# Kernel optimization log

Hardware: AMD Instinct MI355X
Metric: run time of the kernel (lower is better)

The kernel has to match this reference:

```python
import jax, jax.numpy as jnp
import numpy as np

N, D, DH, H = 2048, 256, 256, 4
DHEAD = DH // H
NEG = -1e30


def setup_inputs() -> dict:
    key = jax.random.key(0)
    ks = jax.random.split(key, 24)
    s = 0.05
    inp = {
        'axiom_states': jax.random.normal(ks[0], (N, D), jnp.float32),
        'adj0': (jax.random.uniform(ks[1], (N, N)) < 0.015).astype(jnp.float32),
        'adj1': (jax.random.uniform(ks[2], (N, N)) < 0.015).astype(jnp.float32),
        'w0': jax.random.uniform(ks[3], (N, N), jnp.float32),
        'w1': jax.random.uniform(ks[4], (N, N), jnp.float32),
        'Wm0': jax.random.normal(ks[5], (DH, D), jnp.float32) * s,
        'bm0': jax.random.normal(ks[6], (DH,), jnp.float32) * s,
        'Wa0': jax.random.normal(ks[7], (H, 2 * D), jnp.float32) * s,
        'ba0': jax.random.normal(ks[8], (H,), jnp.float32) * s,
        'Wm1': jax.random.normal(ks[9], (DH, D), jnp.float32) * s,
        'bm1': jax.random.normal(ks[10], (DH,), jnp.float32) * s,
        'Wa1': jax.random.normal(ks[11], (H, 2 * D), jnp.float32) * s,
        'ba1': jax.random.normal(ks[12], (H,), jnp.float32) * s,
        'gru_wih': jax.random.normal(ks[13], (3 * D, 2 * DH), jnp.float32) * s,
        'gru_whh': jax.random.normal(ks[14], (3 * D, D), jnp.float32) * s,
        'gru_bih': jax.random.normal(ks[15], (3 * D,), jnp.float32) * s,
        'gru_bhh': jax.random.normal(ks[16], (3 * D,), jnp.float32) * s,
        'ln_g': jnp.ones((D,), jnp.float32),
        'ln_b': jnp.zeros((D,), jnp.float32),
    }
    return inp


def _edge_messages(x, adj, w, Wm, bm, Wa, ba):
    # GAT-style decomposition of Linear([x_i, x_j]) -> a_cur[i] + a_nb[j] + b
    a_cur = x @ Wa[:, :D].T                      # [N,H] (target i, first half of concat)
    a_nb = x @ Wa[:, D:].T                       # [N,H] (neighbor j, second half)
    s = a_nb[:, None, :] + a_cur[None, :, :] + ba  # [j,i,H]
    s = jax.nn.leaky_relu(s, 0.2)
    s = s * w[:, :, None]                        # edge-weight scaled scores (pre-softmax)
    mask = adj != 0                              # edge j -> i iff adj[j,i] != 0
    logits = jnp.where(mask[:, :, None], s, NEG)
    attn = jax.nn.softmax(logits, axis=0) * mask[:, :, None]  # zero for isolated nodes
    msg = (x @ Wm.T + bm).reshape(N, H, DHEAD)   # per-neighbor messages
    agg = jnp.einsum('jih,jhd->ihd', attn, msg)  # softmax-weighted sum over neighbors
    return agg.reshape(N, DH)


def _forward(axiom_states, adj0, adj1, w0, w1, Wm0, bm0, Wa0, ba0,
             Wm1, bm1, Wa1, ba1, gru_wih, gru_whh, gru_bih, gru_bhh, ln_g, ln_b):
    m0 = _edge_messages(axiom_states, adj0, w0, Wm0, bm0, Wa0, ba0)
    m1 = _edge_messages(axiom_states, adj1, w1, Wm1, bm1, Wa1, ba1)
    msg = jnp.concatenate([m0, m1], axis=-1)     # dropout is identity in eval
    # GRUCell (torch semantics)
    gi = msg @ gru_wih.T + gru_bih
    gh = axiom_states @ gru_whh.T + gru_bhh
    r = jax.nn.sigmoid(gi[:, :D] + gh[:, :D])
    z = jax.nn.sigmoid(gi[:, D:2 * D] + gh[:, D:2 * D])
    n = jnp.tanh(gi[:, 2 * D:] + r * gh[:, 2 * D:])
    h = (1.0 - z) * n + z * axiom_states
    # LayerNorm
    mu = jnp.mean(h, axis=-1, keepdims=True)
    var = jnp.var(h, axis=-1, keepdims=True)
    return (h - mu) * jax.lax.rsqrt(var + 1e-5) * ln_g + ln_b


def reference(axiom_states, adj0, adj1, w0, w1, Wm0, bm0, Wa0, ba0,
              Wm1, bm1, Wa1, ba1, gru_wih, gru_whh, gru_bih, gru_bhh, ln_g, ln_b):
    return _forward(axiom_states, adj0, adj1, w0, w1, Wm0, bm0, Wa0, ba0,
                    Wm1, bm1, Wa1, ba1, gru_wih, gru_whh, gru_bih, gru_bhh, ln_g, ln_b)
```

## Files before the change

kernel.cpp:

```cpp
#include <hip/hip_runtime.h>

#define NN 2048
#define DD 256
#define HH 4
#define ECAP 128

typedef unsigned short ushort_t;
typedef __attribute__((ext_vector_type(4))) unsigned short us4;
typedef __attribute__((ext_vector_type(8))) unsigned short us8;
typedef __attribute__((ext_vector_type(8))) short s8;
typedef __attribute__((ext_vector_type(4))) float f4;

__device__ __forceinline__ ushort_t f2b(float f) {
    unsigned int u = __float_as_uint(f);
    return (ushort_t)((u + 0x7fffu + ((u >> 16) & 1u)) >> 16);
}
__device__ __forceinline__ float b2f(ushort_t b) {
    return __uint_as_float(((unsigned int)b) << 16);
}
__device__ __forceinline__ void gl_lds16(const void* g, void* l) {
    __builtin_amdgcn_global_load_lds(
        (const __attribute__((address_space(1))) void*)g,
        (__attribute__((address_space(3))) void*)l, 16, 0, 0);
}

__device__ __forceinline__ us8 cvt8(float4 a, float4 b) {
    us8 o;
    o[0] = f2b(a.x); o[1] = f2b(a.y); o[2] = f2b(a.z); o[3] = f2b(a.w);
    o[4] = f2b(b.x); o[5] = f2b(b.y); o[6] = f2b(b.z); o[7] = f2b(b.w);
    return o;
}

__device__ __forceinline__ void gemm_core_f32(
    const float* __restrict__ A, int lda, const float* __restrict__ B, int ldb,
    int r0, int c0, int K, ushort_t (*as)[64], ushort_t (*bs)[64], f4 acc[2][2])
{
    const int t = threadIdx.x;
    const int wave = t >> 6, lane = t & 63;
    const int wm = (wave & 1) * 32, wn = (wave >> 1) * 32;
    const int fm = lane & 15, fq = lane >> 4;

    const int m1 = wave * 16 + (lane >> 3);
    const int m2 = m1 + 8;
    const int g1 = ((lane & 7) ^ (m1 & 7)) * 8;
    const int g2 = ((lane & 7) ^ (m2 & 7)) * 8;
    const int cl = (lane & 7) * 8;
    const int ra0 = wm + fm, ra1 = wm + 16 + fm;
    const int rb0 = wn + fm, rb1 = wn + 16 + fm;

    const float* pa1 = A + (size_t)(r0 + m1) * lda + g1;
    const float* pa2 = A + (size_t)(r0 + m2) * lda + g2;
    const float* pb1 = B + (size_t)(c0 + m1) * ldb + g1;
    const float* pb2 = B + (size_t)(c0 + m2) * ldb + g2;

    float4 aa0 = *(const float4*)(pa1);
    float4 aa1 = *(const float4*)(pa1 + 4);
    float4 ab0 = *(const float4*)(pa2);
    float4 ab1 = *(const float4*)(pa2 + 4);
    float4 ba0 = *(const float4*)(pb1);
    float4 ba1 = *(const float4*)(pb1 + 4);
    float4 bb0 = *(const float4*)(pb2);
    float4 bb1 = *(const float4*)(pb2 + 4);

    for (int k0 = 0; k0 < K; k0 += 64) {
        __syncthreads();
        *(us8*)&as[m1][cl] = cvt8(aa0, aa1);
        *(us8*)&as[m2][cl] = cvt8(ab0, ab1);
        *(us8*)&bs[m1][cl] = cvt8(ba0, ba1);
        *(us8*)&bs[m2][cl] = cvt8(bb0, bb1);
        __syncthreads();
        if (k0 + 64 < K) {
            aa0 = *(const float4*)(pa1 + k0 + 64);
            aa1 = *(const float4*)(pa1 + k0 + 68);
            ab0 = *(const float4*)(pa2 + k0 + 64);
            ab1 = *(const float4*)(pa2 + k0 + 68);
            ba0 = *(const float4*)(pb1 + k0 + 64);
            ba1 = *(const float4*)(pb1 + k0 + 68);
            bb0 = *(const float4*)(pb2 + k0 + 64);
            bb1 = *(const float4*)(pb2 + k0 + 68);
        }
        #pragma unroll
        for (int kk = 0; kk < 2; ++kk) {
            const int cc = kk * 4 + fq;
            const s8 a0 = *(const s8*)&as[ra0][(cc ^ (ra0 & 7)) * 8];
            const s8 a1 = *(const s8*)&as[ra1][(cc ^ (ra1 & 7)) * 8];
            const s8 b0 = *(const s8*)&bs[rb0][(cc ^ (rb0 & 7)) * 8];
            const s8 b1 = *(const s8*)&bs[rb1][(cc ^ (rb1 & 7)) * 8];
            acc[0][0] = __builtin_amdgcn_mfma_f32_16x16x32_bf16(a0, b0, acc[0][0], 0, 0, 0);
            acc[0][1] = __builtin_amdgcn_mfma_f32_16x16x32_bf16(a0, b1, acc[0][1], 0, 0, 0);
            acc[1][0] = __builtin_amdgcn_mfma_f32_16x16x32_bf16(a1, b0, acc[1][0], 0, 0, 0);
            acc[1][1] = __builtin_amdgcn_mfma_f32_16x16x32_bf16(a1, b1, acc[1][1], 0, 0, 0);
        }
    }
}

#define E_SC  256
#define E_AP  384
#define E_NB  1024

__global__ __launch_bounds__(256) void fused1_kernel(
    const float* __restrict__ x,
    const float* __restrict__ adj0, const float* __restrict__ adj1,
    const float* __restrict__ Wm0, const float* __restrict__ Wm1,
    const float* __restrict__ whh,
    const float* __restrict__ Wa0, const float* __restrict__ Wa1,
    const float* __restrict__ bm0, const float* __restrict__ bm1,
    const float* __restrict__ bhh,
    int* __restrict__ cnt, int* __restrict__ ej,
    float* __restrict__ acur, float* __restrict__ anb,
    ushort_t* __restrict__ msgb, float* __restrict__ gh)
{
    __shared__ char smem[16448];
    const int b = blockIdx.x, t = threadIdx.x;

    if (b < E_SC) {
        const int l = b & 1, chunk = b >> 1;
        const int i0 = chunk * 16;
        const float* adj = l ? adj1 : adj0;
        int* lcnt = (int*)smem;
        if (t < 16) lcnt[t] = 0;
        __syncthreads();
        const int rowLane = t >> 2, q = t & 3;
        for (int r0r = 0; r0r < NN; r0r += 512) {
            float4 a[8];
            #pragma unroll
            for (int it = 0; it < 8; ++it) {
                const int j = r0r + it * 64 + rowLane;
                a[it] = *(const float4*)(adj + (size_t)j * NN + i0 + q * 4);
            }
            #pragma unroll
            for (int it = 0; it < 8; ++it) {
                const int j = r0r + it * 64 + rowLane;
                const float av[4] = {a[it].x, a[it].y, a[it].z, a[it].w};
                #pragma unroll
                for (int u = 0; u < 4; ++u) {
                    if (av[u] != 0.f) {
                        const int li = q * 4 + u;
                        const int slot = atomicAdd(&lcnt[li], 1);
                        if (slot < ECAP)
                            ej[((size_t)l * NN + i0 + li) * ECAP + slot] = j;
                    }
                }
            }
        }
        __syncthreads();
        if (t < 16) cnt[l * NN + i0 + t] = min(lcnt[t], ECAP);
        return;
    }
    if (b < E_AP) {
        float* sh = (float*)smem;
        const int i0 = (b - E_SC) * 16;
        for (int rr = 0; rr < 16; ++rr)
            sh[rr * 257 + t] = x[(size_t)(i0 + rr) * DD + t];
        __syncthreads();
        const int r = t >> 4, idx = t & 15;
        const int l = idx >> 3, isnb = (idx >> 2) & 1, h = idx & 3;
        const float* wrow = (l ? Wa1 : Wa0) + h * (2 * DD) + isnb * DD;
        float acc = 0.f;
        for (int k = 0; k < DD; ++k) acc = fmaf(sh[r * 257 + k], wrow[k], acc);
        float* dst = isnb ? anb : acur;
        dst[((size_t)l * NN + i0 + r) * HH + h] = acc;
        return;
    }
    {
        ushort_t (*as)[64] = (ushort_t(*)[64])smem;
        ushort_t (*bs)[64] = (ushort_t(*)[64])(smem + 8192);
        const int wave = t >> 6, lane = t & 63;
        const int wm = (wave & 1) * 32, wn = (wave >> 1) * 32;
        const int fm = lane & 15, fq = lane >> 4;
        const int idx = b - E_AP;
        const int c0 = (idx % 20) * 64, r0 = (idx / 20) * 64;
        const float* Bsrc = (c0 < 256) ? Wm0 + (size_t)c0 * DD
                          : (c0 < 512) ? Wm1 + (size_t)(c0 - 256) * DD
                                       : whh + (size_t)(c0 - 512) * DD;
        f4 acc[2][2] = {};
        gemm_core_f32(x, DD, Bsrc, DD, r0, 0, DD, as, bs, acc);
        #pragma unroll
        for (int ni = 0; ni < 2; ++ni) {
            const int col = c0 + wn + ni * 16 + fm;
            const float bv = (col < 256) ? bm0[col]
                           : (col < 512) ? bm1[col - 256]
                                         : bhh[col - 512];
            #pragma unroll
            for (int mi = 0; mi < 2; ++mi) {
                #pragma unroll
                for (int r = 0; r < 4; ++r) {
                    const int row = r0 + wm + mi * 16 + fq * 4 + r;
                    const float v = acc[mi][ni][r] + bv;
                    if (col < 512) msgb[(size_t)row * 512 + col] = f2b(v);
                    else           gh[(size_t)row * 768 + col - 512] = v;
                }
            }
        }
    }
}

__global__ __launch_bounds__(256) void attn_kernel(
    const int* __restrict__ cnt, const int* __restrict__ ej,
    const float* __restrict__ w0, const float* __restrict__ w1,
    const float* __restrict__ acur, const float* __restrict__ anb,
    const float* __restrict__ ba0, const float* __restrict__ ba1,
    const ushort_t* __restrict__ msgb, ushort_t* __restrict__ mcatb,
    const float* __restrict__ wih, ushort_t* __restrict__ wihb)
{
    const int i = blockIdx.x, l = blockIdx.y, t = threadIdx.x;
    __shared__ float es[HH][ECAP];
    __shared__ int ejs[ECAP];

    {
        const int fb = i + (l << 11);
        if (t < 24) {
            const int id = fb * 96 + t * 4;
            const float4 v = *(const float4*)(wih + id);
            us4 o; o.x = f2b(v.x); o.y = f2b(v.y); o.z = f2b(v.z); o.w = f2b(v.w);
            *(us4*)(wihb + id) = o;
        }
    }

    const int ne = min(max(cnt[l * NN + i], 0), ECAP);
    const float* ba = l ? ba1 : ba0;
    const float* w  = l ? w1 : w0;
    const size_t ebase = ((size_t)l * NN + i) * ECAP;

    if (t < ne) {
        const int j = ej[ebase + t];
        const float wv = w[(size_t)j * NN + i];
        ejs[t] = j;
        const float4 av = *(const float4*)(anb + ((size_t)l * NN + j) * HH);
        const float sv[4] = {av.x, av.y, av.z, av.w};
        #pragma unroll
        for (int h = 0; h < HH; ++h) {
            float s = sv[h] + acur[((size_t)l * NN + i) * HH + h] + ba[h];
            s = (s > 0.f) ? s : 0.2f * s;
            es[h][t] = s * wv;
        }
    }
    __syncthreads();
    {
        const int h = t >> 6, lane = t & 63;
        float s0 = (lane < ne) ? es[h][lane] : -1e30f;
        float s1 = (lane + 64 < ne) ? es[h][lane + 64] : -1e30f;
        float m = fmaxf(s0, s1);
        #pragma unroll
        for (int off = 32; off; off >>= 1) m = fmaxf(m, __shfl_xor(m, off));
        const float p0 = expf(s0 - m), p1 = expf(s1 - m);
        float sum = p0 + p1;
        #pragma unroll
        for (int off = 32; off; off >>= 1) sum += __shfl_xor(sum, off);
        const float inv = (ne > 0) ? 1.f / sum : 0.f;
        es[h][lane] = p0 * inv;
        if (lane + 64 < ECAP) es[h][lane + 64] = p1 * inv;
    }
    __syncthreads();
    const int h = t >> 6;
    const int off = l * DD + t;
    float acc = 0.f;
    int e = 0;
    for (; e + 8 <= ne; e += 8) {
        float v[8];
        #pragma unroll
        for (int u = 0; u < 8; ++u)
            v[u] = b2f(msgb[(size_t)ejs[e + u] * 512 + off]);
        #pragma unroll
        for (int u = 0; u < 8; ++u)
            acc = fmaf(es[h][e + u], v[u], acc);
    }
    for (; e < ne; ++e)
        acc = fmaf(es[h][e], b2f(msgb[(size_t)ejs[e] * 512 + off]), acc);
    mcatb[(size_t)i * (2 * DD) + off] = f2b(acc);
}

__global__ __launch_bounds__(256) void gemm2_kernel(
    const ushort_t* __restrict__ mcatb, const ushort_t* __restrict__ wihb,
    const float* __restrict__ bih, float* __restrict__ gi)
{
    __shared__ ushort_t as[256][64];
    __shared__ ushort_t bs[128][64];
    const int t = threadIdx.x;
    const int wave = t >> 6, lane = t & 63;
    const int wm = wave * 32;
    const int fm = lane & 15, fq = lane >> 4;
    const int c0 = blockIdx.x * 64, r0 = blockIdx.y * 128;

    const int lr = lane >> 3;
    const int swz = ((lane & 7) ^ lr) * 8;
    const ushort_t* gaA[4];
    const ushort_t* gaB[2];
    #pragma unroll
    for (int g = 0; g < 4; ++g)
        gaA[g] = mcatb + (size_t)(r0 + wm + g * 8 + lr) * 512 + swz;
    #pragma unroll
    for (int g = 0; g < 2; ++g)
        gaB[g] = wihb + (size_t)(c0 + wave * 16 + g * 8 + lr) * 512 + swz;

    f4 acc[2][4] = {};

    #pragma unroll
    for (int g = 0; g < 4; ++g) gl_lds16(gaA[g], &as[wm + g * 8][0]);
    #pragma unroll
    for (int g = 0; g < 2; ++g) gl_lds16(gaB[g], &bs[wave * 16 + g * 8][0]);
    __syncthreads();

    int abuf = 0, bbuf = 0;
    for (int k0 = 0; k0 < 512; k0 += 64) {
        const int na = abuf ^ 128, nb = bbuf ^ 64;
        if (k0 + 64 < 512) {
            #pragma unroll
            for (int g = 0; g < 4; ++g)
                gl_lds16(gaA[g] + k0 + 64, &as[na + wm + g * 8][0]);
            #pragma unroll
            for (int g = 0; g < 2; ++g)
                gl_lds16(gaB[g] + k0 + 64, &bs[nb + wave * 16 + g * 8][0]);
        }
        #pragma unroll
        for (int kk = 0; kk < 2; ++kk) {
            const int cc = kk * 4 + fq;
            const int ce = (cc ^ (fm & 7)) * 8;
            s8 af[2], bf[4];
            #pragma unroll
            for (int mi = 0; mi < 2; ++mi)
                af[mi] = *(const s8*)&as[abuf + wm + mi * 16 + fm][ce];
            #pragma unroll
            for (int ni = 0; ni < 4; ++ni)
                bf[ni] = *(const s8*)&bs[bbuf + ni * 16 + fm][ce];
            #pragma unroll
            for (int mi = 0; mi < 2; ++mi)
                #pragma unroll
                for (int ni = 0; ni < 4; ++ni)
                    acc[mi][ni] = __builtin_amdgcn_mfma_f32_16x16x32_bf16(
                        af[mi], bf[ni], acc[mi][ni], 0, 0, 0);
        }
        __syncthreads();
        abuf = na; bbuf = nb;
    }
    #pragma unroll
    for (int ni = 0; ni < 4; ++ni) {
        const int col = c0 + ni * 16 + fm;
        const float bv = bih[col];
        #pragma unroll
        for (int mi = 0; mi < 2; ++mi)
            #pragma unroll
            for (int r = 0; r < 4; ++r)
                gi[(size_t)(r0 + wm + mi * 16 + fq * 4 + r) * 768 + col] =
                    acc[mi][ni][r] + bv;
    }
}

__global__ __launch_bounds__(256) void gates_ln(
    const float* __restrict__ gi, const float* __restrict__ gh, const float* __restrict__ x,
    const float* __restrict__ lng, const float* __restrict__ lnb, float* __restrict__ out)
{
    const int t = threadIdx.x;
    const int lane = t & 63, wv = t >> 6;
    const int row = blockIdx.x * 4 + wv;
    const size_t b768 = (size_t)row * 768;
    const int c = lane * 4;
    const f4 gir = *(const f4*)(gi + b768 + c);
    const f4 giz = *(const f4*)(gi + b768 + 256 + c);
    const f4 gin = *(const f4*)(gi + b768 + 512 + c);
    const f4 ghr = *(const f4*)(gh + b768 + c);
    const f4 ghz = *(const f4*)(gh + b768 + 256 + c);
    const f4 ghn = *(const f4*)(gh + b768 + 512 + c);
    const f4 xv  = *(const f4*)(x + (size_t)row * DD + c);
    f4 hv;
    float s1 = 0.f, s2 = 0.f;
    #pragma unroll
    for (int u = 0; u < 4; ++u) {
        const float rr = 1.f / (1.f + expf(-(gir[u] + ghr[u])));
        const float zz = 1.f / (1.f + expf(-(giz[u] + ghz[u])));
        const float nn = tanhf(gin[u] + rr * ghn[u]);
        const float h = (1.f - zz) * nn + zz * xv[u];
        hv[u] = h;
        s1 += h;
        s2 += h * h;
    }
    #pragma unroll
    for (int off = 32; off; off >>= 1) {
        s1 += __shfl_xor(s1, off);
        s2 += __shfl_xor(s2, off);
    }
    const float mu  = s1 * (1.f / DD);
    const float var = s2 * (1.f / DD) - mu * mu;
    const float inv = rsqrtf(var + 1e-5f);
    const f4 gv = *(const f4*)(lng + c);
    const f4 bv = *(const f4*)(lnb + c);
    f4 res;
    #pragma unroll
    for (int u = 0; u < 4; ++u)
        res[u] = (hv[u] - mu) * inv * gv[u] + bv[u];
    *(f4*)(out + (size_t)row * DD + c) = res;
}

extern "C" void kernel_launch(void* const* d_in, const int* in_sizes, int n_in,
                              void* d_out, int out_size, void* d_ws, size_t ws_size,
                              hipStream_t stream)
{
    const float* x    = (const float*)d_in[0];
    const float* adj0 = (const float*)d_in[1];
    const float* adj1 = (const float*)d_in[2];
    const float* w0   = (const float*)d_in[3];
    const float* w1   = (const float*)d_in[4];
    const float* Wm0  = (const float*)d_in[5];
    const float* bm0  = (const float*)d_in[6];
    const float* Wa0  = (const float*)d_in[7];
    const float* ba0  = (const float*)d_in[8];
    const float* Wm1  = (const float*)d_in[9];
    const float* bm1  = (const float*)d_in[10];
    const float* Wa1  = (const float*)d_in[11];
    const float* ba1  = (const float*)d_in[12];
    const float* wih  = (const float*)d_in[13];
    const float* whh  = (const float*)d_in[14];
    const float* bih  = (const float*)d_in[15];
    const float* bhh  = (const float*)d_in[16];
    const float* lng  = (const float*)d_in[17];
    const float* lnb  = (const float*)d_in[18];
    float* out = (float*)d_out;

    float* ws = (float*)d_ws;
    float* gh   = ws;            ws += (size_t)NN * 768;
    float* gi   = ws;            ws += (size_t)NN * 768;
    float* acur = ws;            ws += 2 * NN * HH;
    float* anb  = ws;            ws += 2 * NN * HH;
    int*   cnt  = (int*)ws;      ws += 2 * NN;
    int*   ej   = (int*)ws;      ws += 2 * NN * ECAP;
    ushort_t* wihb  = (ushort_t*)ws;  ws += (size_t)768 * 512 / 2;
    ushort_t* msgb  = (ushort_t*)ws;  ws += (size_t)NN * 512 / 2;
    ushort_t* mcatb = (ushort_t*)ws;  ws += (size_t)NN * 512 / 2;

    fused1_kernel<<<E_NB, 256, 0, stream>>>(
        x, adj0, adj1, Wm0, Wm1, whh, Wa0, Wa1, bm0, bm1, bhh,
        cnt, ej, acur, anb, msgb, gh);
    attn_kernel<<<dim3(NN, 2), 256, 0, stream>>>(
        cnt, ej, w0, w1, acur, anb, ba0, ba1, msgb, mcatb, wih, wihb);
    gemm2_kernel<<<dim3(12, 16), 256, 0, stream>>>(mcatb, wihb, bih, gi);
    gates_ln<<<NN / 4, 256, 0, stream>>>(gi, gh, x, lng, lnb, out);
}
```

Baseline: 167.6 us.

## Split adjacency scan over four row quarters with per-quarter edge lists

The adjacency scan in the fused first kernel is split across four blocks per column chunk, each handling 512 source rows, giving four times as many scan blocks. Each quarter writes its own edge list and count. The attention kernel rebuilds the combined neighbor list by prefix-summing the four counts and indexing into the right quarter. This raises parallelism for the memory-bound scan of both 16 MB adjacency matrices, at the cost of a little extra index math and a per-quarter cap that could drop edges if one quarter holds more than 64.

After: 168.5 us. No clear change (+0.6%).

```diff
diff --git a/kernel.cpp b/kernel.cpp
--- a/kernel.cpp
+++ b/kernel.cpp
@@ -4,6 +4,7 @@
 #define DD 256
 #define HH 4
 #define ECAP 128
+#define QCAP 64
 
 typedef unsigned short ushort_t;
 typedef __attribute__((ext_vector_type(4))) unsigned short us4;
@@ -94,9 +95,9 @@
     }
 }
 
-#define E_SC  256
-#define E_AP  384
-#define E_NB  1024
+#define E_SC  1024
+#define E_AP  1152
+#define E_NB  1792
 
 __global__ __launch_bounds__(256) void fused1_kernel(
     const float* __restrict__ x,
@@ -106,7 +107,7 @@
     const float* __restrict__ Wa0, const float* __restrict__ Wa1,
     const float* __restrict__ bm0, const float* __restrict__ bm1,
     const float* __restrict__ bhh,
-    int* __restrict__ cnt, int* __restrict__ ej,
+    int* __restrict__ cntq, int* __restrict__ ej4,
     float* __restrict__ acur, float* __restrict__ anb,
     ushort_t* __restrict__ msgb, float* __restrict__ gh)
 {
@@ -114,37 +115,41 @@
     const int b = blockIdx.x, t = threadIdx.x;
 
     if (b < E_SC) {
-        const int l = b & 1, chunk = b >> 1;
+        const int l = b & 1;
+        const int c2 = b >> 1;
+        const int chunk = c2 & 127;
+        const int qt = c2 >> 7;
         const int i0 = chunk * 16;
+        const int jbase = qt * 512;
+        const int qp = qt * 2 + l;
         const float* adj = l ? adj1 : adj0;
         int* lcnt = (int*)smem;
         if (t < 16) lcnt[t] = 0;
         __syncthreads();
         const int rowLane = t >> 2, q = t & 3;
-        for (int r0r = 0; r0r < NN; r0r += 512) {
-            float4 a[8];
-            #pragma unroll
-            for (int it = 0; it < 8; ++it) {
-                const int j = r0r + it * 64 + rowLane;
-                a[it] = *(const float4*)(adj + (size_t)j * NN + i0 + q * 4);
-            }
-            #pragma unroll
-            for (int it = 0; it < 8; ++it) {
-                const int j = r0r + it * 64 + rowLane;
-                const float av[4] = {a[it].x, a[it].y, a[it].z, a[it].w};
-                #pragma unroll
-                for (int u = 0; u < 4; ++u) {
-                    if (av[u] != 0.f) {
-                        const int li = q * 4 + u;
-                        const int slot = atomicAdd(&lcnt[li], 1);
-                        if (slot < ECAP)
-                            ej[((size_t)l * NN + i0 + li) * ECAP + slot] = j;
-                    }
+        float4 a[8];
+        #pragma unroll
+        for (int it = 0; it < 8; ++it) {
+            const int j = jbase + it * 64 + rowLane;
+            a[it] = *(const float4*)(adj + (size_t)j * NN + i0 + q * 4);
+        }
+        #pragma unroll
+        for (int it = 0; it < 8; ++it) {
+            const int j = jbase + it * 64 + rowLane;
+            const float av[4] = {a[it].x, a[it].y, a[it].z, a[it].w};
+            #pragma unroll
+            for (int u = 0; u < 4; ++u) {
+                if (av[u] != 0.f) {
+                    const int li = q * 4 + u;
+                    const int slot = atomicAdd(&lcnt[li], 1);
+                    if (slot < QCAP)
+                        ej4[((size_t)qp * NN + i0 + li) * QCAP + slot] = j;
                 }
             }
         }
         __syncthreads();
-        if (t < 16) cnt[l * NN + i0 + t] = min(lcnt[t], ECAP);
+        if (t < 16)
+            cntq[((size_t)qp * 128 + chunk) * 32 + t] = min(lcnt[t], QCAP);
         return;
     }
     if (b < E_AP) {
@@ -196,7 +201,7 @@
 }
 
 __global__ __launch_bounds__(256) void attn_kernel(
-    const int* __restrict__ cnt, const int* __restrict__ ej,
+    const int* __restrict__ cntq, const int* __restrict__ ej4,
     const float* __restrict__ w0, const float* __restrict__ w1,
     const float* __restrict__ acur, const float* __restrict__ anb,
     const float* __restrict__ ba0, const float* __restrict__ ba1,
@@ -217,13 +222,20 @@
         }
     }
 
-    const int ne = min(max(cnt[l * NN + i], 0), ECAP);
+    const int chunk = i >> 4, li = i & 15;
+    const int n0 = cntq[((size_t)(0 * 2 + l) * 128 + chunk) * 32 + li];
+    const int n1 = cntq[((size_t)(1 * 2 + l) * 128 + chunk) * 32 + li];
+    const int n2 = cntq[((size_t)(2 * 2 + l) * 128 + chunk) * 32 + li];
+    const int n3 = cntq[((size_t)(3 * 2 + l) * 128 + chunk) * 32 + li];
+    const int P1 = n0, P2 = n0 + n1, P3 = n0 + n1 + n2;
+    const int ne = min(P3 + n3, ECAP);
     const float* ba = l ? ba1 : ba0;
     const float* w  = l ? w1 : w0;
-    const size_t ebase = ((size_t)l * NN + i) * ECAP;
 
     if (t < ne) {
-        const int j = ej[ebase + t];
+        const int qt = (t >= P1) + (t >= P2) + (t >= P3);
+        const int off = t - (qt == 0 ? 0 : (qt == 1 ? P1 : (qt == 2 ? P2 : P3)));
+        const int j = ej4[((size_t)(qt * 2 + l) * NN + i) * QCAP + off];
         const float wv = w[(size_t)j * NN + i];
         ejs[t] = j;
         const float4 av = *(const float4*)(anb + ((size_t)l * NN + j) * HH);
@@ -421,17 +433,17 @@
     float* gi   = ws;            ws += (size_t)NN * 768;
     float* acur = ws;            ws += 2 * NN * HH;
     float* anb  = ws;            ws += 2 * NN * HH;
-    int*   cnt  = (int*)ws;      ws += 2 * NN;
-    int*   ej   = (int*)ws;      ws += 2 * NN * ECAP;
+    int*   cntq = (int*)ws;      ws += 8 * 128 * 32;
+    int*   ej4  = (int*)ws;      ws += (size_t)8 * NN * QCAP;
     ushort_t* wihb  = (ushort_t*)ws;  ws += (size_t)768 * 512 / 2;
     ushort_t* msgb  = (ushort_t*)ws;  ws += (size_t)NN * 512 / 2;
     ushort_t* mcatb = (ushort_t*)ws;  ws += (size_t)NN * 512 / 2;
 
     fused1_kernel<<<E_NB, 256, 0, stream>>>(
         x, adj0, adj1, Wm0, Wm1, whh, Wa0, Wa1, bm0, bm1, bhh,
-        cnt, ej, acur, anb, msgb, gh);
+        cntq, ej4, acur, anb, msgb, gh);
     attn_kernel<<<dim3(NN, 2), 256, 0, stream>>>(
-        cnt, ej, w0, w1, acur, anb, ba0, ba1, msgb, mcatb, wih, wihb);
+        cntq, ej4, w0, w1, acur, anb, ba0, ba1, msgb, mcatb, wih, wihb);
     gemm2_kernel<<<dim3(12, 16), 256, 0, stream>>>(mcatb, wihb, bih, gi);
     gates_ln<<<NN / 4, 256, 0, stream>>>(gi, gh, x, lng, lnb, out);
 }
```
